# Performance work log

Measured on AMD Instinct MI355X. Metric: run time of the kernel, lower is better.

The kernel has to match this reference:

```python
import jax, jax.numpy as jnp
import numpy as np

N, E, D, L = 50000, 800000, 128, 2
EPS = 1e-10


def mobius_add(x, y, c):
    # c: shape [1], broadcasts against [N,1]
    xy = jnp.sum(x * y, axis=-1, keepdims=True)
    x2 = jnp.sum(x * x, axis=-1, keepdims=True)
    y2 = jnp.sum(y * y, axis=-1, keepdims=True)
    num = (1 + 2 * c * xy + c * y2) * x + (1 - c * x2) * y
    den = 1 + 2 * c * xy + (c ** 2) * x2 * y2
    return num / den


def log_map(x, y, c):
    ym = mobius_add(-x, y, c)
    n = jnp.maximum(jnp.linalg.norm(ym, axis=-1, keepdims=True), EPS)
    sc = jnp.sqrt(c)
    return (2.0 / sc) * jnp.arctanh(sc * n) * ym / n


def exp_map(x, v, c):
    n = jnp.maximum(jnp.linalg.norm(v, axis=-1, keepdims=True), EPS)
    sc = jnp.sqrt(c)
    second = jnp.tanh(sc * n / 2.0) * v / (sc * n)
    return mobius_add(x, second, c)


def l2norm(x):
    return x / jnp.maximum(jnp.linalg.norm(x, axis=-1, keepdims=True), 1e-12)


def mean_agg(h, src, dst, n_nodes):
    # copy_u + mean reduce: mean of h[src] grouped by dst; zero-degree -> 0
    msum = jax.ops.segment_sum(h[src], dst, num_segments=n_nodes)
    deg = jax.ops.segment_sum(jnp.ones((src.shape[0], 1), h.dtype), dst, num_segments=n_nodes)
    return msum / jnp.maximum(deg, 1.0)


def setup_inputs() -> dict:
    key = jax.random.key(0)
    ks = jax.random.split(key, 12)
    scale = 1.0 / np.sqrt(D)
    return {
        "src": jax.random.randint(ks[0], (E,), 0, N, dtype=jnp.int32),
        "dst": jax.random.randint(ks[1], (E,), 0, N, dtype=jnp.int32),
        "e_emb": jax.random.normal(ks[2], (N, D), dtype=jnp.float32),
        "b_emb": 0.01 * jax.random.normal(ks[3], (N, D), dtype=jnp.float32),  # inside Poincare ball
        "s_emb": jax.random.normal(ks[4], (N, D), dtype=jnp.float32),
        "e_W": scale * jax.random.normal(ks[5], (L, D, D), dtype=jnp.float32),
        "e_b": jnp.zeros((L, D), dtype=jnp.float32),
        "b_W": scale * jax.random.normal(ks[6], (L, D, D), dtype=jnp.float32),
        "b_b": jnp.zeros((L, D), dtype=jnp.float32),
        "s_W": scale * jax.random.normal(ks[7], (L, D, D), dtype=jnp.float32),
        "s_b": jnp.zeros((L, D), dtype=jnp.float32),
        "b_curvature": jnp.ones((1,), dtype=jnp.float32),
        "s_curvature": jnp.ones((1,), dtype=jnp.float32),
    }


def reference(src, dst, e_emb, b_emb, s_emb, e_W, e_b, b_W, b_b, s_W, s_b, b_curvature, s_curvature):
    n = e_emb.shape[0]
    origin = jnp.zeros((1, b_emb.shape[-1]), dtype=b_emb.dtype)
    for l in range(L):
        # Euclidean: transform -> mean aggregate -> LeakyReLU(0.2)
        h = e_emb @ e_W[l].T + e_b[l]
        e_emb = mean_agg(h, src, dst, n)
        e_emb = jnp.where(e_emb > 0, e_emb, 0.2 * e_emb)
        # Hyperbolic: log map to tangent -> transform -> mean aggregate -> exp map
        tangent = log_map(origin, b_emb, b_curvature)
        hb = tangent @ b_W[l].T + b_b[l]
        neigh_b = mean_agg(hb, src, dst, n)
        b_emb = exp_map(origin, neigh_b, b_curvature)
        # Spherical: normalize -> transform -> normalize -> mean aggregate -> normalize
        hs = l2norm(l2norm(s_emb) @ s_W[l].T + s_b[l])
        s_emb = l2norm(mean_agg(hs, src, dst, n))
    return (e_emb, b_emb, s_emb)
```

## Files before the change

### kernel.cpp

```cpp
#include <hip/hip_runtime.h>
#include <math.h>

#define DD 128
typedef unsigned int   u32;
typedef unsigned short u16;
typedef short bf16x8 __attribute__((ext_vector_type(8)));
typedef float f32x4  __attribute__((ext_vector_type(4)));

__device__ __forceinline__ float lo2f(u32 p){ return __uint_as_float(p << 16); }
__device__ __forceinline__ float hi2f(u32 p){ return __uint_as_float(p & 0xFFFF0000u); }
__device__ __forceinline__ u16 f2bf(float f){
    u32 u = __float_as_uint(f);
    return (u16)((u + 0x7fffu + ((u >> 16) & 1u)) >> 16);
}

__global__ void k_hist(const int* __restrict__ dst, int* __restrict__ deg, int E){
    int i = blockIdx.x*256 + threadIdx.x;
    if (i < E) atomicAdd(&deg[dst[i]], 1);
}

__global__ void k_chunksum(const int* __restrict__ deg, int* __restrict__ csum,
                           float* __restrict__ invdeg, int n){
    __shared__ int sdata[256];
    int t = threadIdx.x;
    int i0 = blockIdx.x*512 + t*2;
    int a = (i0     < n) ? deg[i0]   : 0;
    int b = (i0 + 1 < n) ? deg[i0+1] : 0;
    if (i0     < n) invdeg[i0]   = 1.0f / (float)max(a, 1);
    if (i0 + 1 < n) invdeg[i0+1] = 1.0f / (float)max(b, 1);
    sdata[t] = a + b; __syncthreads();
    for (int off = 128; off > 0; off >>= 1){
        if (t < off) sdata[t] += sdata[t+off];
        __syncthreads();
    }
    if (t == 0) csum[blockIdx.x] = sdata[0];
}

__global__ void k_scanchunks(int* __restrict__ csum, int nchunks,
                             int* __restrict__ row_ptr, int n){
    __shared__ int s[256];
    __shared__ int carry_sh;
    int t = threadIdx.x;
    if (t == 0) carry_sh = 0;
    __syncthreads();
    for (int base = 0; base < nchunks; base += 256){
        int i = base + t;
        int v = (i < nchunks) ? csum[i] : 0;
        s[t] = v;
        __syncthreads();
        for (int off = 1; off < 256; off <<= 1){
            int u = (t >= off) ? s[t-off] : 0;
            __syncthreads();
            s[t] += u;
            __syncthreads();
        }
        int carry = carry_sh;
        int excl  = carry + s[t] - v;
        if (i < nchunks) csum[i] = excl;
        int tot = s[255];
        __syncthreads();
        if (t == 0) carry_sh = carry + tot;
        __syncthreads();
    }
    if (t == 0) row_ptr[n] = carry_sh;
}

__global__ void k_scanwithin(const int* __restrict__ deg, const int* __restrict__ csum,
                             int* __restrict__ row_ptr, int* __restrict__ cursor, int n){
    __shared__ int s[256];
    int t = threadIdx.x;
    int i0 = blockIdx.x*512 + t*2;
    int a = (i0     < n) ? deg[i0]   : 0;
    int b = (i0 + 1 < n) ? deg[i0+1] : 0;
    int tsum = a + b;
    s[t] = tsum; __syncthreads();
    for (int off = 1; off < 256; off <<= 1){
        int v = (t >= off) ? s[t-off] : 0;
        __syncthreads();
        s[t] += v;
        __syncthreads();
    }
    int excl = s[t] - tsum + csum[blockIdx.x];
    if (i0     < n){ row_ptr[i0]   = excl;     cursor[i0]   = excl;     }
    if (i0 + 1 < n){ row_ptr[i0+1] = excl + a; cursor[i0+1] = excl + a; }
}

__global__ void k_fill(const int* __restrict__ src, const int* __restrict__ dst,
                       int* __restrict__ cursor, int* __restrict__ sorted_src, int E){
    int i = blockIdx.x*256 + threadIdx.x;
    if (i < E){
        int p = atomicAdd(&cursor[dst[i]], 1);
        sorted_src[p] = src[i];
    }
}

__global__ void k_w2b3(const float* __restrict__ w0, const float* __restrict__ w1,
                       const float* __restrict__ w2,
                       u16* __restrict__ o0, u16* __restrict__ o1, u16* __restrict__ o2,
                       int nw){
    int i = blockIdx.x*256 + threadIdx.x;
    if (i >= nw) return;
    const float* s = (blockIdx.y == 0) ? w0 : (blockIdx.y == 1) ? w1 : w2;
    u16*         o = (blockIdx.y == 0) ? o0 : (blockIdx.y == 1) ? o1 : o2;
    o[i] = f2bf(s[i]);
}

template<int PRE, int POST>
__device__ __forceinline__ void gemm_body(const float* __restrict__ X, const u16* __restrict__ Wb,
                                          const float* __restrict__ bias, u16* __restrict__ Y,
                                          size_t sstride, int n_rows, const float* __restrict__ cptr){
    int t = threadIdx.x;
    int wave = t >> 6, lane = t & 63;
    int q = lane >> 4, m = lane & 15;
    int rowbase = blockIdx.x*64 + wave*16;
    int gr = min(rowbase + m, n_rows - 1);

    float4 xv[8];
    const float4* xp = (const float4*)(X + (size_t)gr*DD);
    #pragma unroll
    for (int c = 0; c < 4; c++){
        xv[2*c]   = xp[c*8 + q*2];
        xv[2*c+1] = xp[c*8 + q*2 + 1];
    }

    float scale = 1.0f;
    if (PRE != 0){
        float ss = 0.f;
        #pragma unroll
        for (int i = 0; i < 8; i++)
            ss += xv[i].x*xv[i].x + xv[i].y*xv[i].y + xv[i].z*xv[i].z + xv[i].w*xv[i].w;
        ss += __shfl_xor(ss, 16, 64);
        ss += __shfl_xor(ss, 32, 64);
        float nrm = sqrtf(ss);
        if (PRE == 1){
            float c  = cptr[0];
            c = (c > 0.f && c < 1e30f) ? c : 1.0f;
            float sc = sqrtf(c);
            float n2 = fmaxf(nrm, 1e-10f);
            float a  = fminf(sc*n2, 0.99999994f);
            scale = (2.0f/sc) * atanhf(a) / n2;
        } else {
            scale = 1.0f / fmaxf(nrm, 1e-12f);
        }
    }

    bf16x8 af[4];
    #pragma unroll
    for (int c = 0; c < 4; c++){
        const float* xf = (const float*)&xv[2*c];
        #pragma unroll
        for (int j = 0; j < 8; j++) af[c][j] = (short)f2bf(xf[j]*scale);
    }

    f32x4 acc[8];
    #pragma unroll
    for (int tl = 0; tl < 8; tl++) acc[tl] = (f32x4){0.f,0.f,0.f,0.f};

    const u16* wb = Wb + (size_t)m*DD + q*8;
    #pragma unroll
    for (int c = 0; c < 4; c++){
        #pragma unroll
        for (int tl = 0; tl < 8; tl++){
            bf16x8 bfr = *(const bf16x8*)(wb + (size_t)tl*16*DD + c*32);
            acc[tl] = __builtin_amdgcn_mfma_f32_16x16x32_bf16(af[c], bfr, acc[tl], 0, 0, 0);
        }
    }

    #pragma unroll
    for (int tl = 0; tl < 8; tl++){
        float bv = bias[tl*16 + m];
        #pragma unroll
        for (int r = 0; r < 4; r++) acc[tl][r] += bv;
    }
    if (POST == 1){
        float ssr[4] = {0.f,0.f,0.f,0.f};
        #pragma unroll
        for (int tl = 0; tl < 8; tl++)
            #pragma unroll
            for (int r = 0; r < 4; r++) ssr[r] += acc[tl][r]*acc[tl][r];
        #pragma unroll
        for (int r = 0; r < 4; r++){
            float s = ssr[r];
            s += __shfl_xor(s, 1, 64);
            s += __shfl_xor(s, 2, 64);
            s += __shfl_xor(s, 4, 64);
            s += __shfl_xor(s, 8, 64);
            float sc = 1.0f / fmaxf(sqrtf(s), 1e-12f);
            #pragma unroll
            for (int tl = 0; tl < 8; tl++) acc[tl][r] *= sc;
        }
    }
    #pragma unroll
    for (int r = 0; r < 4; r++){
        int grow = rowbase + q*4 + r;
        if (grow < n_rows){
            #pragma unroll
            for (int tl = 0; tl < 8; tl++)
                Y[(size_t)(tl>>1)*sstride + (size_t)grow*32 + (tl&1)*16 + m] = f2bf(acc[tl][r]);
        }
    }
}

template<int PREB>
__global__ __launch_bounds__(256, 4)
void k_gemm3(const float* __restrict__ Xe, const float* __restrict__ Xb, const float* __restrict__ Xs,
             const u16* __restrict__ We, const u16* __restrict__ Wh, const u16* __restrict__ Ws,
             const float* __restrict__ be, const float* __restrict__ bb, const float* __restrict__ bs,
             u16* __restrict__ ebS, u16* __restrict__ sS,
             int n_rows, const float* __restrict__ cptr){
    size_t sstride = (size_t)n_rows * 32;
    if (blockIdx.y == 0)      gemm_body<0,0>(Xe, We, be, ebS,            sstride, n_rows, cptr);
    else if (blockIdx.y == 1) gemm_body<PREB,0>(Xb, Wh, bb, ebS+4*sstride, sstride, n_rows, cptr);
    else                      gemm_body<2,1>(Xs, Ws, bs, sS,             sstride, n_rows, cptr);
}

#define NPG 2
__device__ __forceinline__ void acc8(float* a, uint4 p){
    a[0] += lo2f(p.x); a[1] += hi2f(p.x);
    a[2] += lo2f(p.y); a[3] += hi2f(p.y);
    a[4] += lo2f(p.z); a[5] += hi2f(p.z);
    a[6] += lo2f(p.w); a[7] += hi2f(p.w);
}

__global__ __launch_bounds__(256)
void k_aggT(const u32* __restrict__ ebS, const u32* __restrict__ sS,
            const int* __restrict__ row_ptr, const int* __restrict__ sorted_src,
            const float* __restrict__ invdeg,
            float* __restrict__ oE, float* __restrict__ oB, float* __restrict__ oS,
            int n_rows){
    const int NPB = 64*NPG;
    int xcd = blockIdx.x & 7;
    int idx = blockIdx.x >> 3;
    int nbE = (n_rows + NPB - 1) / NPB;
    size_t sstride = (size_t)n_rows * 16;

    const u32* shard; float* dest; int nodebase, hi, colbase; bool leaky;
    if (idx < nbE){
        int c = xcd;
        shard = ebS + (size_t)c * sstride;
        dest = (c < 4) ? oE : oB;
        leaky = (c < 4);
        colbase = (c & 3) * 32;
        nodebase = idx * NPB; hi = n_rows;
    } else {
        int half = xcd >> 2, c = xcd & 3;
        int lo  = (int)(((long long)n_rows * half) >> 1);
        int hi2 = (int)(((long long)n_rows * (half+1)) >> 1);
        int nbS = (hi2 - lo + NPB - 1) / NPB;
        int i2 = idx - nbE;
        if (i2 >= nbS) return;
        shard = sS + (size_t)c * sstride;
        dest = oS; leaky = false;
        colbase = c * 32;
        nodebase = lo + i2*NPB; hi = hi2;
    }

    int grp = threadIdx.x >> 2;
    int l4  = threadIdx.x & 3;
    const u32* tbl = shard + l4*4;

    #pragma unroll
    for (int k = 0; k < NPG; k++){
        int v = nodebase + k*64 + grp;
        if (v >= hi) continue;
        int beg = row_ptr[v], end = row_ptr[v+1];
        float a[8];
        #pragma unroll
        for (int i = 0; i < 8; i++) a[i] = 0.f;

        int p = beg;
        for (; p + 1 < end; p += 2){
            int i0 = sorted_src[p];
            int i1 = sorted_src[p+1];
            uint4 c0 = *(const uint4*)(tbl + (size_t)i0*16);
            uint4 c1 = *(const uint4*)(tbl + (size_t)i1*16);
            acc8(a, c0); acc8(a, c1);
        }
        if (p < end){
            int i0 = sorted_src[p];
            uint4 c0 = *(const uint4*)(tbl + (size_t)i0*16);
            acc8(a, c0);
        }

        float inv = invdeg[v];
        f32x4 o0, o1;
        #pragma unroll
        for (int i = 0; i < 4; i++){
            float x = a[i]*inv;
            o0[i] = (leaky && x < 0.f) ? 0.2f*x : x;
        }
        #pragma unroll
        for (int i = 0; i < 4; i++){
            float x = a[4+i]*inv;
            o1[i] = (leaky && x < 0.f) ? 0.2f*x : x;
        }
        f32x4* dp = (f32x4*)(dest + (size_t)v*DD + colbase + l4*8);
        __builtin_nontemporal_store(o0, dp);
        __builtin_nontemporal_store(o1, dp+1);
    }
}

__global__ __launch_bounds__(256)
void k_final(const float* __restrict__ tb, const float* __restrict__ ts,
             float* __restrict__ ob, float* __restrict__ os,
             int n_rows, const float* __restrict__ cptr){
    int wid = (blockIdx.x*256 + threadIdx.x) >> 6;
    if (wid >= n_rows) return;
    int lane = threadIdx.x & 63;
    float2 vb = *(const float2*)(tb + (size_t)wid*DD + lane*2);
    float2 vs = *(const float2*)(ts + (size_t)wid*DD + lane*2);
    float ssb = vb.x*vb.x + vb.y*vb.y;
    float sss = vs.x*vs.x + vs.y*vs.y;
    #pragma unroll
    for (int m = 32; m > 0; m >>= 1){
        ssb += __shfl_xor(ssb, m, 64);
        sss += __shfl_xor(sss, m, 64);
    }
    float cc = cptr[0];
    cc = (cc > 0.f && cc < 1e30f) ? cc : 1.0f;
    float sc = sqrtf(cc);
    float nb = fmaxf(sqrtf(ssb), 1e-10f);
    float scb = tanhf(sc*nb*0.5f) / (sc*nb);
    float scs = 1.0f / fmaxf(sqrtf(sss), 1e-12f);
    *(float2*)(ob + (size_t)wid*DD + lane*2) = make_float2(vb.x*scb, vb.y*scb);
    *(float2*)(os + (size_t)wid*DD + lane*2) = make_float2(vs.x*scs, vs.y*scs);
}

extern "C" void kernel_launch(void* const* d_in, const int* in_sizes, int n_in,
                              void* d_out, int out_size, void* d_ws, size_t ws_size,
                              hipStream_t stream){
    const int*   src = (const int*)d_in[0];
    const int*   dst = (const int*)d_in[1];
    const float* emb_in[3] = {(const float*)d_in[2], (const float*)d_in[3], (const float*)d_in[4]};
    const float* W_in[3]   = {(const float*)d_in[5], (const float*)d_in[7], (const float*)d_in[9]};
    const float* b_in[3]   = {(const float*)d_in[6], (const float*)d_in[8], (const float*)d_in[10]};
    const float* b_c       = (const float*)d_in[11];

    const int E  = in_sizes[0];
    const int ND = in_sizes[2];
    const int N  = ND / DD;
    const int Lnum = in_sizes[5] / (DD*DD);
    const int nw = Lnum*DD*DD;
    const int nchunks = (N + 511) / 512;

    char* w = (char*)d_ws;
    auto alloc = [&](size_t bytes)->char*{
        char* p = w; w += (bytes + 255) & ~(size_t)255; return p;
    };
    u32*   ebS       = (u32*)  alloc((size_t)ND*4);
    u32*   sS        = (u32*)  alloc((size_t)ND*2);
    float* tb        = (float*)alloc((size_t)ND*4);
    float* ts        = (float*)alloc((size_t)ND*4);
    u16*   Wb[3];
    for (int i = 0; i < 3; i++) Wb[i] = (u16*)alloc((size_t)nw*2);
    float* invdeg    = (float*)alloc((size_t)N*4);
    int*   deg       = (int*)  alloc((size_t)N*4);
    int*   row_ptr   = (int*)  alloc((size_t)(N+1)*4);
    int*   cursor    = (int*)  alloc((size_t)N*4);
    int*   csum      = (int*)  alloc((size_t)nchunks*4);
    int*   sorted_src= (int*)  alloc((size_t)E*4);
    (void)ws_size; (void)n_in; (void)out_size;

    float* out_e = (float*)d_out;
    float* out_b = out_e + ND;
    float* out_s = out_e + 2*ND;

    hipMemsetAsync(deg, 0, (size_t)N*4, stream);

    const int TB = 256;
    k_w2b3<<<dim3((nw+TB-1)/TB, 3), TB, 0, stream>>>(W_in[0], W_in[1], W_in[2],
                                                     Wb[0], Wb[1], Wb[2], nw);
    k_hist<<<(E+TB-1)/TB, TB, 0, stream>>>(dst, deg, E);
    k_chunksum<<<nchunks, 256, 0, stream>>>(deg, csum, invdeg, N);
    k_scanchunks<<<1, 256, 0, stream>>>(csum, nchunks, row_ptr, N);
    k_scanwithin<<<nchunks, 256, 0, stream>>>(deg, csum, row_ptr, cursor, N);
    k_fill<<<(E+TB-1)/TB, TB, 0, stream>>>(src, dst, cursor, sorted_src, E);

    const int gemmblocks = (N + 63) / 64;
    const int NPB = 64*NPG;
    const int nbE = (N + NPB - 1) / NPB;
    const int nbS = (((N + 1) / 2) + NPB - 1) / NPB;
    const int aggblocks = 8 * (nbE + nbS);
    const int finblocks = (N + 3) / 4;

    const float* se = emb_in[0];
    const float* sb = emb_in[1];
    const float* ss = emb_in[2];

    for (int l = 0; l < Lnum; l++){
        bool last = (l == Lnum - 1);
        if (l == 0)
            k_gemm3<1><<<dim3(gemmblocks, 3), 256, 0, stream>>>(
                se, sb, ss,
                Wb[0] + (size_t)l*DD*DD, Wb[1] + (size_t)l*DD*DD, Wb[2] + (size_t)l*DD*DD,
                b_in[0] + (size_t)l*DD,  b_in[1] + (size_t)l*DD,  b_in[2] + (size_t)l*DD,
                (u16*)ebS, (u16*)sS, N, b_c);
        else
            k_gemm3<0><<<dim3(gemmblocks, 3), 256, 0, stream>>>(
                se, sb, ss,
                Wb[0] + (size_t)l*DD*DD, Wb[1] + (size_t)l*DD*DD, Wb[2] + (size_t)l*DD*DD,
                b_in[0] + (size_t)l*DD,  b_in[1] + (size_t)l*DD,  b_in[2] + (size_t)l*DD,
                (u16*)ebS, (u16*)sS, N, b_c);

        float* dB = last ? tb : out_b;
        float* dS = last ? ts : out_s;
        k_aggT<<<aggblocks, 256, 0, stream>>>(ebS, sS, row_ptr, sorted_src, invdeg,
                                              out_e, dB, dS, N);
        if (last)
            k_final<<<finblocks, 256, 0, stream>>>(tb, ts, out_b, out_s, N, b_c);

        se = out_e; sb = out_b; ss = out_s;
    }
}
```

Before: 542.1 us.

## Use 16-bit edge indices, prefetch 4-wide gathers, split aggregation kernel by table

When the node count fits in 16 bits, the CSR source index array is stored as u16, which halves the index bytes read during aggregation. The gather loop is unrolled four-wide, and the next four indices are prefetched while the current four row loads are in flight, to hide index-load latency. The single combined aggregation launch is split into two template-specialised launches, one for the Euclidean/hyperbolic table and one for the spherical table, which removes per-block branching but adds a kernel launch per layer.

```diff
diff --git a/kernel.cpp b/kernel.cpp
--- a/kernel.cpp
+++ b/kernel.cpp
@@ -85,12 +85,13 @@
     if (i0 + 1 < n){ row_ptr[i0+1] = excl + a; cursor[i0+1] = excl + a; }
 }
 
+template<typename IT>
 __global__ void k_fill(const int* __restrict__ src, const int* __restrict__ dst,
-                       int* __restrict__ cursor, int* __restrict__ sorted_src, int E){
+                       int* __restrict__ cursor, IT* __restrict__ sorted_src, int E){
     int i = blockIdx.x*256 + threadIdx.x;
     if (i < E){
         int p = atomicAdd(&cursor[dst[i]], 1);
-        sorted_src[p] = src[i];
+        sorted_src[p] = (IT)src[i];
     }
 }
 
@@ -222,37 +223,35 @@
     a[6] += lo2f(p.w); a[7] += hi2f(p.w);
 }
 
+template<typename IT, int MODE>
 __global__ __launch_bounds__(256)
-void k_aggT(const u32* __restrict__ ebS, const u32* __restrict__ sS,
-            const int* __restrict__ row_ptr, const int* __restrict__ sorted_src,
+void k_aggT(const u32* __restrict__ tab,
+            const int* __restrict__ row_ptr, const IT* __restrict__ sorted_src,
             const float* __restrict__ invdeg,
             float* __restrict__ oE, float* __restrict__ oB, float* __restrict__ oS,
             int n_rows){
     const int NPB = 64*NPG;
     int xcd = blockIdx.x & 7;
     int idx = blockIdx.x >> 3;
-    int nbE = (n_rows + NPB - 1) / NPB;
     size_t sstride = (size_t)n_rows * 16;
 
     const u32* shard; float* dest; int nodebase, hi, colbase; bool leaky;
-    if (idx < nbE){
-        int c = xcd;
-        shard = ebS + (size_t)c * sstride;
-        dest = (c < 4) ? oE : oB;
-        leaky = (c < 4);
-        colbase = (c & 3) * 32;
+    if (MODE == 0){
+        shard = tab + (size_t)xcd * sstride;
+        dest = (xcd < 4) ? oE : oB;
+        leaky = (xcd < 4);
+        colbase = (xcd & 3) * 32;
         nodebase = idx * NPB; hi = n_rows;
+        if (nodebase >= hi) return;
     } else {
         int half = xcd >> 2, c = xcd & 3;
         int lo  = (int)(((long long)n_rows * half) >> 1);
         int hi2 = (int)(((long long)n_rows * (half+1)) >> 1);
-        int nbS = (hi2 - lo + NPB - 1) / NPB;
-        int i2 = idx - nbE;
-        if (i2 >= nbS) return;
-        shard = sS + (size_t)c * sstride;
+        shard = tab + (size_t)c * sstride;
         dest = oS; leaky = false;
         colbase = c * 32;
-        nodebase = lo + i2*NPB; hi = hi2;
+        nodebase = lo + idx*NPB; hi = hi2;
+        if (nodebase >= hi) return;
     }
 
     int grp = threadIdx.x >> 2;
@@ -264,21 +263,35 @@
         int v = nodebase + k*64 + grp;
         if (v >= hi) continue;
         int beg = row_ptr[v], end = row_ptr[v+1];
+        int cnt = end - beg;
         float a[8];
         #pragma unroll
         for (int i = 0; i < 8; i++) a[i] = 0.f;
 
+        int nq = cnt >> 2;
         int p = beg;
-        for (; p + 1 < end; p += 2){
-            int i0 = sorted_src[p];
-            int i1 = sorted_src[p+1];
-            uint4 c0 = *(const uint4*)(tbl + (size_t)i0*16);
-            uint4 c1 = *(const uint4*)(tbl + (size_t)i1*16);
-            acc8(a, c0); acc8(a, c1);
-        }
-        if (p < end){
-            int i0 = sorted_src[p];
-            uint4 c0 = *(const uint4*)(tbl + (size_t)i0*16);
+        int j0 = 0, j1 = 0, j2 = 0, j3 = 0;
+        if (nq > 0){
+            j0 = (int)sorted_src[p]; j1 = (int)sorted_src[p+1];
+            j2 = (int)sorted_src[p+2]; j3 = (int)sorted_src[p+3];
+        }
+        for (int q = 0; q < nq; q++){
+            uint4 c0 = *(const uint4*)(tbl + (size_t)j0*16);
+            uint4 c1 = *(const uint4*)(tbl + (size_t)j1*16);
+            uint4 c2 = *(const uint4*)(tbl + (size_t)j2*16);
+            uint4 c3 = *(const uint4*)(tbl + (size_t)j3*16);
+            p += 4;
+            if (q + 1 < nq){
+                j0 = (int)sorted_src[p];
+                j1 = (int)sorted_src[p+1];
+                j2 = (int)sorted_src[p+2];
+                j3 = (int)sorted_src[p+3];
+            }
+            acc8(a, c0); acc8(a, c1); acc8(a, c2); acc8(a, c3);
+        }
+        for (int r = 0; r < (cnt & 3); r++){
+            int j = (int)sorted_src[p + r];
+            uint4 c0 = *(const uint4*)(tbl + (size_t)j*16);
             acc8(a, c0);
         }
 
@@ -342,6 +355,7 @@
     const int Lnum = in_sizes[5] / (DD*DD);
     const int nw = Lnum*DD*DD;
     const int nchunks = (N + 511) / 512;
+    const bool small_idx = (N <= 65535);
 
     char* w = (char*)d_ws;
     auto alloc = [&](size_t bytes)->char*{
@@ -358,7 +372,7 @@
     int*   row_ptr   = (int*)  alloc((size_t)(N+1)*4);
     int*   cursor    = (int*)  alloc((size_t)N*4);
     int*   csum      = (int*)  alloc((size_t)nchunks*4);
-    int*   sorted_src= (int*)  alloc((size_t)E*4);
+    void*  sorted_src= (void*) alloc((size_t)E*4);
     (void)ws_size; (void)n_in; (void)out_size;
 
     float* out_e = (float*)d_out;
@@ -374,13 +388,15 @@
     k_chunksum<<<nchunks, 256, 0, stream>>>(deg, csum, invdeg, N);
     k_scanchunks<<<1, 256, 0, stream>>>(csum, nchunks, row_ptr, N);
     k_scanwithin<<<nchunks, 256, 0, stream>>>(deg, csum, row_ptr, cursor, N);
-    k_fill<<<(E+TB-1)/TB, TB, 0, stream>>>(src, dst, cursor, sorted_src, E);
+    if (small_idx)
+        k_fill<u16><<<(E+TB-1)/TB, TB, 0, stream>>>(src, dst, cursor, (u16*)sorted_src, E);
+    else
+        k_fill<int><<<(E+TB-1)/TB, TB, 0, stream>>>(src, dst, cursor, (int*)sorted_src, E);
 
     const int gemmblocks = (N + 63) / 64;
     const int NPB = 64*NPG;
     const int nbE = (N + NPB - 1) / NPB;
     const int nbS = (((N + 1) / 2) + NPB - 1) / NPB;
-    const int aggblocks = 8 * (nbE + nbS);
     const int finblocks = (N + 3) / 4;
 
     const float* se = emb_in[0];
@@ -404,8 +420,17 @@
 
         float* dB = last ? tb : out_b;
         float* dS = last ? ts : out_s;
-        k_aggT<<<aggblocks, 256, 0, stream>>>(ebS, sS, row_ptr, sorted_src, invdeg,
-                                              out_e, dB, dS, N);
+        if (small_idx){
+            k_aggT<u16,0><<<8*nbE, 256, 0, stream>>>(ebS, row_ptr, (const u16*)sorted_src,
+                                                     invdeg, out_e, dB, dS, N);
+            k_aggT<u16,1><<<8*nbS, 256, 0, stream>>>(sS,  row_ptr, (const u16*)sorted_src,
+                                                     invdeg, out_e, dB, dS, N);
+        } else {
+            k_aggT<int,0><<<8*nbE, 256, 0, stream>>>(ebS, row_ptr, (const int*)sorted_src,
+                                                     invdeg, out_e, dB, dS, N);
+            k_aggT<int,1><<<8*nbS, 256, 0, stream>>>(sS,  row_ptr, (const int*)sorted_src,
+                                                     invdeg, out_e, dB, dS, N);
+        }
         if (last)
             k_final<<<finblocks, 256, 0, stream>>>(tb, ts, out_b, out_s, N, b_c);
 
```

Result: faster. 495.7 us (-8.6%).
